# Performance work log

Measured on AMD Instinct MI355X. Metric: run time of the kernel, lower is better.

The kernel has to match this reference:

```python
import jax, jax.numpy as jnp
import numpy as np

N = 100000      # nodes
E = 1600000     # edges
G = 1024        # graphs in batch
H = 128         # graph_hidden
F_IN = 38
DEPTH = 4
EPS = 1e-5


def setup_inputs() -> dict:
    key = jax.random.key(0)
    ks = jax.random.split(key, 16)
    inp = {
        "h": jax.random.normal(ks[0], (N, F_IN), jnp.float32),
        "src": jax.random.randint(ks[1], (E,), 0, N, jnp.int32),
        "dst": jax.random.randint(ks[2], (E,), 0, N, jnp.int32),
        "node2graph": jnp.sort(jax.random.randint(ks[3], (N,), 0, G, jnp.int32)),
        "W1": jax.random.normal(ks[4], (F_IN, H), jnp.float32) * 0.1,
        "b1": jnp.zeros((H,), jnp.float32),
        "g1": jnp.ones((H,), jnp.float32),
        "be1": jnp.zeros((H,), jnp.float32),
        "W2s": jax.random.normal(ks[5], (DEPTH - 1, H, H), jnp.float32) * 0.1,
        "b2s": jnp.zeros((DEPTH - 1, H), jnp.float32),
        "g2s": jnp.ones((DEPTH - 1, H), jnp.float32),
        "be2s": jnp.zeros((DEPTH - 1, H), jnp.float32),
        "aw": jax.random.normal(ks[6], (H, 1), jnp.float32) * 0.1,
        "ab": jnp.zeros((1,), jnp.float32),
        "Wf1": jax.random.normal(ks[7], (H, 512), jnp.float32) * 0.1,
        "bf1": jnp.zeros((512,), jnp.float32),
        "gf1": jnp.ones((512,), jnp.float32),
        "bef1": jnp.zeros((512,), jnp.float32),
        "Wl": jax.random.normal(ks[8], (512, 256), jnp.float32) * 0.05,
        "bl": jnp.zeros((256,), jnp.float32),
        "gl": jnp.ones((256,), jnp.float32),
        "bel": jnp.zeros((256,), jnp.float32),
        "Wf2": jax.random.normal(ks[9], (256, 67), jnp.float32) * 0.05,
        "bf2": jnp.zeros((67,), jnp.float32),
    }
    return inp


def _bn(x, g, b):
    # BatchNorm1d in training mode: batch stats (biased variance), eps=1e-5.
    m = jnp.mean(x, axis=0)
    v = jnp.mean(jnp.square(x - m), axis=0)
    return g * (x - m) * jax.lax.rsqrt(v + EPS) + b


def reference(h, src, dst, node2graph,
              W1, b1, g1, be1, W2s, b2s, g2s, be2s,
              aw, ab, Wf1, bf1, gf1, bef1, Wl, bl, gl, bel, Wf2, bf2):
    ones_e = jnp.ones((E,), h.dtype)
    deg_out = jax.ops.segment_sum(ones_e, src, num_segments=N)
    deg_in = jax.ops.segment_sum(ones_e, dst, num_segments=N)
    ns = jax.lax.rsqrt(jnp.maximum(deg_out, 1.0))  # src-side D^{-1/2}
    nd = jax.lax.rsqrt(jnp.maximum(deg_in, 1.0))   # dst-side D^{-1/2}

    def gconv(x, W, b):
        # DGL GraphConv norm='both': D_dst^{-1/2} A D_src^{-1/2} x W + b
        msg = (x * ns[:, None])[src]                      # [E, F] gather
        agg = jax.ops.segment_sum(msg, dst, num_segments=N)
        return (agg * nd[:, None]) @ W + b

    # dropout p = 0.0 -> identity
    x = jax.nn.relu(_bn(gconv(h, W1, b1), g1, be1))
    for i in range(DEPTH - 1):
        x = jax.nn.relu(_bn(gconv(x, W2s[i], b2s[i]), g2s[i], be2s[i]))

    # WeightAndSum readout: sigmoid-gated segment sum over nodes per graph
    atom_weights = x @ aw + ab                            # [N, 1] (pre-sigmoid, returned)
    w = jax.nn.sigmoid(atom_weights)
    hg = jax.ops.segment_sum(x * w, node2graph, num_segments=G)  # [G, H]

    y = jax.nn.relu(_bn(hg @ Wf1 + bf1, gf1, bef1))
    y = jax.nn.relu(_bn(y @ Wl + bl, gl, bel))
    y = jax.nn.sigmoid(y @ Wf2 + bf2)                     # [G, 67]
    return (y, atom_weights)
```

## Files before the change

### kernel.cpp

```cpp
#include <hip/hip_runtime.h>
#include <math.h>

#define NN 100000
#define NE 1600000
#define NG 1024
#define MAXDEG 64
#define EPSB 1e-5f

#define NBUK 1563
#define NBLK 256
#define EPB  6250
#define FLAT (2*NBUK*NBLK)
#define NCH  ((FLAT + 1023)/1024)

typedef _Float16 h16;
typedef __attribute__((ext_vector_type(2))) _Float16 h16x2;
typedef __attribute__((ext_vector_type(4))) _Float16 h16x4;
typedef __attribute__((ext_vector_type(8))) _Float16 h16x8;
typedef __attribute__((ext_vector_type(4))) float f32x4;

static __device__ __forceinline__ float sigmoidf_(float x){ return 1.f/(1.f+__expf(-x)); }

__global__ __launch_bounds__(256)
void k_hist(const int* __restrict__ src, const int* __restrict__ dst,
            int* __restrict__ blockHist){
  __shared__ int hd[NBUK];
  __shared__ int hs[NBUK];
  int b = blockIdx.x, t = threadIdx.x;
  for (int j = t; j < NBUK; j += 256){ hd[j] = 0; hs[j] = 0; }
  __syncthreads();
  int e0 = b*EPB, e1 = e0 + EPB;
  for (int i = e0 + t; i < e1; i += 256){
    atomicAdd(&hd[dst[i]>>6], 1);
    atomicAdd(&hs[src[i]>>6], 1);
  }
  __syncthreads();
  for (int j = t; j < NBUK; j += 256){
    blockHist[(size_t)j*NBLK + b] = hd[j];
    blockHist[(size_t)(NBUK + j)*NBLK + b] = hs[j];
  }
}

__global__ __launch_bounds__(256)
void k_scan1(int* __restrict__ data, int* __restrict__ csum){
  __shared__ int s[256];
  int blk = blockIdx.x, t = threadIdx.x;
  int base = blk*1024 + t*4;
  int v0=0,v1=0,v2=0,v3=0;
  if (base+0 < FLAT) v0 = data[base+0];
  if (base+1 < FLAT) v1 = data[base+1];
  if (base+2 < FLAT) v2 = data[base+2];
  if (base+3 < FLAT) v3 = data[base+3];
  int tot = v0+v1+v2+v3;
  s[t] = tot; __syncthreads();
  for (int o=1;o<256;o<<=1){ int x = (t>=o)? s[t-o]:0; __syncthreads(); s[t]+=x; __syncthreads(); }
  int excl = s[t] - tot;
  if (t == 255) csum[blk] = s[255];
  if (base+0 < FLAT) data[base+0] = excl;
  if (base+1 < FLAT) data[base+1] = excl + v0;
  if (base+2 < FLAT) data[base+2] = excl + v0 + v1;
  if (base+3 < FLAT) data[base+3] = excl + v0 + v1 + v2;
}

__global__ void k_scan2(int* __restrict__ csum){
  __shared__ int s[1024];
  int t = threadIdx.x;
  int x = (t < NCH) ? csum[t] : 0;
  s[t] = x; __syncthreads();
  for (int o=1;o<1024;o<<=1){ int y = (t>=o)? s[t-o]:0; __syncthreads(); s[t]+=y; __syncthreads(); }
  if (t < NCH) csum[t] = s[t] - x;
}

__global__ __launch_bounds__(256)
void k_scan3(int* __restrict__ data, const int* __restrict__ csum){
  int blk = blockIdx.x, t = threadIdx.x;
  int add = csum[blk];
  int base = blk*1024 + t*4;
  if (base+0 < FLAT) data[base+0] += add;
  if (base+1 < FLAT) data[base+1] += add;
  if (base+2 < FLAT) data[base+2] += add;
  if (base+3 < FLAT) data[base+3] += add;
}

__global__ __launch_bounds__(256)
void k_scatter(const int* __restrict__ src, const int* __restrict__ dst,
               const int* __restrict__ scanned, unsigned int* __restrict__ sortedBuf){
  __shared__ int bd[NBUK];
  __shared__ int bs[NBUK];
  int b = blockIdx.x, t = threadIdx.x;
  for (int j = t; j < NBUK; j += 256){
    bd[j] = scanned[(size_t)j*NBLK + b];
    bs[j] = scanned[(size_t)(NBUK + j)*NBLK + b];
  }
  __syncthreads();
  int e0 = b*EPB, e1 = e0 + EPB;
  for (int i = e0 + t; i < e1; i += 256){
    int s = src[i], d = dst[i];
    int posD = atomicAdd(&bd[d>>6], 1);
    sortedBuf[posD] = (unsigned int)s | ((unsigned int)(d & 63) << 20);
    int posS = atomicAdd(&bs[s>>6], 1);
    sortedBuf[posS] = (unsigned int)s;
  }
}

__global__ __launch_bounds__(256)
void k_build(const unsigned int* __restrict__ sortedBuf, const int* __restrict__ scanned,
             int* __restrict__ eidx, int* __restrict__ degI,
             float* __restrict__ ns, float* __restrict__ nd){
  __shared__ int cnt[64];
  int k = blockIdx.x, t = threadIdx.x;
  int v0 = k*64;
  int nv = NN - v0; if (nv > 64) nv = 64;
  if (t < 64) cnt[t] = 0;
  __syncthreads();
  int startD = scanned[(size_t)k*NBLK];
  int endD   = scanned[(size_t)(k+1)*NBLK];
  for (int i = startD + t; i < endD; i += 256){
    unsigned int u = sortedBuf[i];
    int lid = (int)(u >> 20);
    int slot = atomicAdd(&cnt[lid], 1);
    if (slot < MAXDEG) eidx[(size_t)(v0 + lid)*MAXDEG + slot] = (int)(u & 0xFFFFFu);
  }
  __syncthreads();
  if (t < nv){
    int v = v0 + t;
    int dI = cnt[t];
    degI[v] = dI;
    nd[v] = rsqrtf(fmaxf((float)dI, 1.f));
    int c = dI > MAXDEG ? MAXDEG : dI;
    int ad = (c + 7) & ~7; if (ad < 8) ad = 8; if (ad > MAXDEG) ad = MAXDEG;
    for (int i = c; i < ad; i++) eidx[(size_t)v*MAXDEG + i] = NN;
  }
  __syncthreads();
  if (t < 64) cnt[t] = 0;
  __syncthreads();
  int startS = scanned[(size_t)(NBUK + k)*NBLK];
  int endS   = (k+1 < NBUK) ? scanned[(size_t)(NBUK + k + 1)*NBLK] : 2*NE;
  for (int i = startS + t; i < endS; i += 256){
    atomicAdd(&cnt[sortedBuf[i] & 63u], 1);
  }
  __syncthreads();
  if (t < nv) ns[v0 + t] = rsqrtf(fmaxf((float)cnt[t], 1.f));
}

__global__ void k_prepg(const int* __restrict__ n2g,
                        int* __restrict__ gs, int* __restrict__ ge, float* __restrict__ stats,
                        float* __restrict__ ns, h16* __restrict__ XA, h16* __restrict__ XB){
  int v = blockIdx.x*256 + threadIdx.x;
  if (v < NN){
    int g = n2g[v];
    if (v == 0){
      for (int q = 0; q <= g; q++) gs[q] = 0;
      for (int q = 0; q < g; q++) ge[q] = 0;
    } else {
      int gp = n2g[v-1];
      if (gp != g){
        for (int q = gp+1; q <= g; q++) gs[q] = v;
        for (int q = gp; q < g; q++) ge[q] = v;
      }
    }
    if (v == NN-1){
      for (int q = g+1; q < NG; q++) gs[q] = NN;
      for (int q = g; q < NG; q++) ge[q] = NN;
    }
  }
  if (v == NN) ns[NN] = 0.f;
  if (blockIdx.x == 0){
    int t = threadIdx.x;
    for (int j = t; j < 4096; j += 256) stats[j] = 0.f;
    if (t < 128){ XA[(size_t)NN*128 + t] = (h16)0.f; XB[(size_t)NN*128 + t] = (h16)0.f; }
  }
}

__global__ void k_convall(const float* __restrict__ W1, const float* __restrict__ W2s,
                          const float* __restrict__ Wf1, const float* __restrict__ Wl,
                          h16* __restrict__ W1t, h16* __restrict__ W2t,
                          h16* __restrict__ Wf1t, h16* __restrict__ Wlt){
  int i = blockIdx.x*256 + threadIdx.x;
  if (i < 8192){
    int c = i >> 6, k = i & 63;
    W1t[i] = (k < 38) ? (h16)W1[(size_t)k*128 + c] : (h16)0.f;
  } else if (i < 57344){
    int j = i - 8192; int l = j >> 14; int r = j & 16383;
    int c = r >> 7, k = r & 127;
    W2t[j] = (h16)W2s[(size_t)l*16384 + (size_t)k*128 + c];
  } else if (i < 122880){
    int j = i - 57344; int c = j >> 7, k = j & 127;
    Wf1t[j] = (h16)Wf1[(size_t)k*512 + c];
  } else if (i < 253952){
    int j = i - 122880; int c = j >> 9, k = j & 511;
    Wlt[j] = (h16)Wl[(size_t)k*256 + c];
  }
}

__global__ void k_prep1(const float* __restrict__ h, const float* __restrict__ ns,
                        h16* __restrict__ hn){
  int i = blockIdx.x*256 + threadIdx.x;
  if (i >= (NN+1)*40) return;
  int v = i / 40, c = i - v*40;
  float val = (v < NN && c < 38) ? h[(size_t)v*38 + c]*ns[v] : 0.f;
  hn[i] = (h16)val;
}

__global__ __launch_bounds__(256)
void k_gs40(const h16* __restrict__ hn, const int* __restrict__ eidx,
            const int* __restrict__ degI, const float* __restrict__ nd,
            h16* __restrict__ A38){
  int v = (blockIdx.x*256 + threadIdx.x) >> 6;
  int lane = threadIdx.x & 63;
  if (v >= NN) return;
  int deg = degI[v]; if (deg > MAXDEG) deg = MAXDEG;
  int deg8 = (deg + 7) & ~7; if (deg8 < 8) deg8 = 8; if (deg8 > MAXDEG) deg8 = MAXDEG;
  const int* row = eidx + v*MAXDEG;
  int g = lane / 20;
  int c0 = 2*(lane % 20);
  bool act = (lane < 40);
  int gg = g & 1;
  float a0 = 0.f, a1 = 0.f;
  int4 s4 = *(const int4*)(row + 4*gg);
  h16x2 u0={}, u1={}, u2={}, u3={};
  if (act){
    u0 = *(const h16x2*)(hn + (size_t)s4.x*40 + c0);
    u1 = *(const h16x2*)(hn + (size_t)s4.y*40 + c0);
    u2 = *(const h16x2*)(hn + (size_t)s4.z*40 + c0);
    u3 = *(const h16x2*)(hn + (size_t)s4.w*40 + c0);
  }
  for (int e = 0; e < deg8; e += 8){
    int nx = (e + 8 < deg8) ? e + 8 : e;
    int4 s4n = *(const int4*)(row + nx + 4*gg);
    h16x2 n0={}, n1={}, n2={}, n3={};
    if (act){
      n0 = *(const h16x2*)(hn + (size_t)s4n.x*40 + c0);
      n1 = *(const h16x2*)(hn + (size_t)s4n.y*40 + c0);
      n2 = *(const h16x2*)(hn + (size_t)s4n.z*40 + c0);
      n3 = *(const h16x2*)(hn + (size_t)s4n.w*40 + c0);
    }
    a0 += ((float)u0[0] + (float)u1[0]) + ((float)u2[0] + (float)u3[0]);
    a1 += ((float)u0[1] + (float)u1[1]) + ((float)u2[1] + (float)u3[1]);
    u0=n0; u1=n1; u2=n2; u3=n3;
  }
  float b0 = __shfl(a0, lane + 20);
  float b1 = __shfl(a1, lane + 20);
  if (lane < 20){
    float ndv = nd[v];
    h16x2 o; o[0] = (h16)((a0 + b0)*ndv); o[1] = (h16)((a1 + b1)*ndv);
    *(h16x2*)(A38 + (size_t)v*64 + c0) = o;
  } else if (lane < 32){
    h16x2 o; o[0] = (h16)0.f; o[1] = (h16)0.f;
    *(h16x2*)(A38 + (size_t)v*64 + 40 + 2*(lane - 20)) = o;
  }
}

__global__ __launch_bounds__(256)
void k_gs128(const h16* __restrict__ X, const int* __restrict__ eidx,
             const int* __restrict__ degI, const float* __restrict__ ns,
             const float* __restrict__ nd, const float* __restrict__ stats,
             const float* __restrict__ gam, const float* __restrict__ bet,
             h16* __restrict__ agg){
  __shared__ float scs[128], shs[128];
  int t = threadIdx.x;
  if (t < 128){
    float m = stats[t]*(1.f/(float)NN);
    float var = fmaxf(stats[128+t]*(1.f/(float)NN) - m*m, 0.f);
    float inv = rsqrtf(var + EPSB);
    float sc = gam[t]*inv;
    scs[t] = sc; shs[t] = fmaf(-sc, m, bet[t]);
  }
  __syncthreads();
  int v = (blockIdx.x*256 + t) >> 6;
  int lane = t & 63;
  if (v >= NN) return;
  int deg = degI[v]; if (deg > MAXDEG) deg = MAXDEG;
  int deg8 = (deg + 7) & ~7; if (deg8 < 8) deg8 = 8; if (deg8 > MAXDEG) deg8 = MAXDEG;
  const int* row = eidx + v*MAXDEG;
  int half = lane >> 5;
  int c0 = 4*(lane & 31);
  float4 sc = *(const float4*)&scs[c0];
  float4 sh = *(const float4*)&shs[c0];
  float a0=0.f, a1=0.f, a2=0.f, a3=0.f;
  int4 s4 = *(const int4*)(row + 4*half);
  float w0=ns[s4.x], w1=ns[s4.y], w2=ns[s4.z], w3=ns[s4.w];
  h16x4 u0 = *(const h16x4*)(X + (size_t)s4.x*128 + c0);
  h16x4 u1 = *(const h16x4*)(X + (size_t)s4.y*128 + c0);
  h16x4 u2 = *(const h16x4*)(X + (size_t)s4.z*128 + c0);
  h16x4 u3 = *(const h16x4*)(X + (size_t)s4.w*128 + c0);
  for (int e = 0; e < deg8; e += 8){
    int nx = (e + 8 < deg8) ? e + 8 : e;
    int4 s4n = *(const int4*)(row + nx + 4*half);
    float v0=ns[s4n.x], v1=ns[s4n.y], v2=ns[s4n.z], v3=ns[s4n.w];
    h16x4 n0 = *(const h16x4*)(X + (size_t)s4n.x*128 + c0);
    h16x4 n1 = *(const h16x4*)(X + (size_t)s4n.y*128 + c0);
    h16x4 n2 = *(const h16x4*)(X + (size_t)s4n.z*128 + c0);
    h16x4 n3 = *(const h16x4*)(X + (size_t)s4n.w*128 + c0);
    a0 = fmaf(fmaxf(fmaf((float)u0[0], sc.x, sh.x), 0.f), w0, a0);
    a1 = fmaf(fmaxf(fmaf((float)u0[1], sc.y, sh.y), 0.f), w0, a1);
    a2 = fmaf(fmaxf(fmaf((float)u0[2], sc.z, sh.z), 0.f), w0, a2);
    a3 = fmaf(fmaxf(fmaf((float)u0[3], sc.w, sh.w), 0.f), w0, a3);
    a0 = fmaf(fmaxf(fmaf((float)u1[0], sc.x, sh.x), 0.f), w1, a0);
    a1 = fmaf(fmaxf(fmaf((float)u1[1], sc.y, sh.y), 0.f), w1, a1);
    a2 = fmaf(fmaxf(fmaf((float)u1[2], sc.z, sh.z), 0.f), w1, a2);
    a3 = fmaf(fmaxf(fmaf((float)u1[3], sc.w, sh.w), 0.f), w1, a3);
    a0 = fmaf(fmaxf(fmaf((float)u2[0], sc.x, sh.x), 0.f), w2, a0);
    a1 = fmaf(fmaxf(fmaf((float)u2[1], sc.y, sh.y), 0.f), w2, a1);
    a2 = fmaf(fmaxf(fmaf((float)u2[2], sc.z, sh.z), 0.f), w2, a2);
    a3 = fmaf(fmaxf(fmaf((float)u2[3], sc.w, sh.w), 0.f), w2, a3);
    a0 = fmaf(fmaxf(fmaf((float)u3[0], sc.x, sh.x), 0.f), w3, a0);
    a1 = fmaf(fmaxf(fmaf((float)u3[1], sc.y, sh.y), 0.f), w3, a1);
    a2 = fmaf(fmaxf(fmaf((float)u3[2], sc.z, sh.z), 0.f), w3, a2);
    a3 = fmaf(fmaxf(fmaf((float)u3[3], sc.w, sh.w), 0.f), w3, a3);
    u0=n0; u1=n1; u2=n2; u3=n3;
    w0=v0; w1=v1; w2=v2; w3=v3;
  }
  a0 += __shfl_xor(a0, 32);
  a1 += __shfl_xor(a1, 32);
  a2 += __shfl_xor(a2, 32);
  a3 += __shfl_xor(a3, 32);
  if (half == 0){
    float ndv = nd[v];
    h16x4 o;
    o[0] = (h16)(a0*ndv); o[1] = (h16)(a1*ndv);
    o[2] = (h16)(a2*ndv); o[3] = (h16)(a3*ndv);
    *(h16x4*)(agg + (size_t)v*128 + c0) = o;
  }
}

__global__ __launch_bounds__(256)
void k_mgemm(const h16* __restrict__ A, const h16* __restrict__ Wt,
             const float* __restrict__ bias, h16* __restrict__ Cout,
             float* __restrict__ stats, int M, int K, int Nc){
  __shared__ h16 As[128][72];
  __shared__ h16 Bs[128][72];
  __shared__ float sred[2][128];
  int m0 = blockIdx.x*128, n0 = blockIdx.y*128;
  int t = threadIdx.x, w = t>>6, lane = t&63;
  int wr = (w>>1)*64, wc = (w&1)*64;
  f32x4 acc[4][4] = {};

  int ar = t>>3;
  int ac = (t&7)*8;
  for (int k0=0; k0<K; k0+=64){
    #pragma unroll
    for (int rr=0; rr<128; rr+=32){
      int gm = m0 + ar + rr;
      h16x8 val = {};
      if (gm < M) val = *(const h16x8*)(A + (size_t)gm*K + k0 + ac);
      *(h16x8*)&As[ar+rr][ac] = val;
    }
    #pragma unroll
    for (int rr=0; rr<128; rr+=32){
      int gc = n0 + ar + rr;
      h16x8 val = {};
      if (gc < Nc) val = *(const h16x8*)(Wt + (size_t)gc*K + k0 + ac);
      *(h16x8*)&Bs[ar+rr][ac] = val;
    }
    __syncthreads();
    int rsel = lane & 15;
    #pragma unroll
    for (int kk=0; kk<64; kk+=32){
      int ksel = kk + (lane>>4)*8;
      h16x8 af[4], bfr[4];
      #pragma unroll
      for (int i=0;i<4;i++) af[i]  = *(const h16x8*)&As[wr + i*16 + rsel][ksel];
      #pragma unroll
      for (int j=0;j<4;j++) bfr[j] = *(const h16x8*)&Bs[wc + j*16 + rsel][ksel];
      #pragma unroll
      for (int i=0;i<4;i++)
        #pragma unroll
        for (int j=0;j<4;j++)
          acc[i][j] = __builtin_amdgcn_mfma_f32_16x16x32_f16(af[i], bfr[j], acc[i][j], 0, 0, 0);
    }
    __syncthreads();
  }

  float csum[4] = {}, csq[4] = {};
  int colsel = lane & 15, rowsel = (lane>>4)*4;
  #pragma unroll
  for (int j=0;j<4;j++){
    int gc = n0 + wc + j*16 + colsel;
    float bv = (gc < Nc) ? bias[gc] : 0.f;
    #pragma unroll
    for (int i=0;i<4;i++){
      #pragma unroll
      for (int r=0;r<4;r++){
        int gm = m0 + wr + i*16 + rowsel + r;
        if (gm < M && gc < Nc){
          float v = acc[i][j][r] + bv;
          Cout[(size_t)gm*Nc + gc] = (h16)v;
          csum[j] += v; csq[j] += v*v;
        }
      }
    }
  }
  if (stats){
    ((float*)sred)[t] = 0.f;
    __syncthreads();
    #pragma unroll
    for (int j=0;j<4;j++){
      int lc = wc + j*16 + colsel;
      atomicAdd(&sred[0][lc], csum[j]);
      atomicAdd(&sred[1][lc], csq[j]);
    }
    __syncthreads();
    if (t < 128){
      int gc = n0 + t;
      if (gc < Nc){
        atomicAdd(&stats[gc],      sred[0][t]);
        atomicAdd(&stats[Nc + gc], sred[1][t]);
      }
    }
  }
}

__global__ __launch_bounds__(256)
void k_readout(const h16* __restrict__ X, const float* __restrict__ stats,
               const float* __restrict__ gam, const float* __restrict__ bet,
               const float* __restrict__ aw, const float* __restrict__ ab,
               const int* __restrict__ gs, const int* __restrict__ ge,
               float* __restrict__ awout, h16* __restrict__ hg){
  __shared__ float scs[128], shs[128], awv[128];
  __shared__ float red[4][128];
  int t = threadIdx.x;
  if (t < 128){
    float m = stats[t]*(1.f/(float)NN);
    float var = fmaxf(stats[128+t]*(1.f/(float)NN) - m*m, 0.f);
    float inv = rsqrtf(var + EPSB);
    float sc = gam[t]*inv;
    scs[t] = sc; shs[t] = fmaf(-sc, m, bet[t]);
    awv[t] = aw[t];
  }
  __syncthreads();
  int g = blockIdx.x;
  int s = gs[g], e = ge[g];
  int w = t>>6, lane = t&63, c0 = 2*lane;
  float sc0=scs[c0], sc1=scs[c0+1], sh0=shs[c0], sh1=shs[c0+1];
  float aw0=awv[c0], aw1=awv[c0+1];
  float ab0 = ab[0];
  float acc0=0.f, acc1=0.f;
  for (int n = s + w; n < e; n += 4){
    h16x2 u = *(const h16x2*)(X + (size_t)n*128 + c0);
    float x0 = fmaxf(fmaf((float)u[0], sc0, sh0), 0.f);
    float x1 = fmaxf(fmaf((float)u[1], sc1, sh1), 0.f);
    float d = x0*aw0 + x1*aw1;
    #pragma unroll
    for (int o=32;o>0;o>>=1) d += __shfl_xor(d, o);
    float tv = d + ab0;
    if (lane == 0) awout[n] = tv;
    float wn = sigmoidf_(tv);
    acc0 = fmaf(x0, wn, acc0);
    acc1 = fmaf(x1, wn, acc1);
  }
  red[w][c0] = acc0; red[w][c0+1] = acc1;
  __syncthreads();
  if (w == 0){
    float a0 = red[0][c0] + red[1][c0] + red[2][c0] + red[3][c0];
    float a1 = red[0][c0+1] + red[1][c0+1] + red[2][c0+1] + red[3][c0+1];
    h16x2 o; o[0] = (h16)a0; o[1] = (h16)a1;
    *(h16x2*)(hg + (size_t)g*128 + c0) = o;
  }
}

__global__ __launch_bounds__(256)
void k_bnapply_f(const h16* __restrict__ X, h16* __restrict__ Y,
                 const float* __restrict__ stats, const float* __restrict__ gam,
                 const float* __restrict__ bet, float invM, int C, int totalPairs){
  __shared__ float scs[512], shs[512];
  int t = threadIdx.x;
  for (int c = t; c < C; c += 256){
    float m = stats[c]*invM;
    float var = fmaxf(stats[C+c]*invM - m*m, 0.f);
    float inv = rsqrtf(var + EPSB);
    float sc = gam[c]*inv;
    scs[c] = sc; shs[c] = fmaf(-sc, m, bet[c]);
  }
  __syncthreads();
  int i = blockIdx.x*256 + t;
  if (i >= totalPairs) return;
  int pm = (C >> 1) - 1;
  int c0 = 2*(i & pm);
  h16x2 u = *(const h16x2*)(X + 2*(size_t)i);
  float x0 = fmaxf(fmaf((float)u[0], scs[c0],   shs[c0]),   0.f);
  float x1 = fmaxf(fmaf((float)u[1], scs[c0+1], shs[c0+1]), 0.f);
  h16x2 o; o[0] = (h16)x0; o[1] = (h16)x1;
  *(h16x2*)(Y + 2*(size_t)i) = o;
}

__global__ void k_final(const h16* __restrict__ y2, const float* __restrict__ Wf2,
                        const float* __restrict__ bf2v, float* __restrict__ out){
  int idx = blockIdx.x*256 + threadIdx.x;
  if (idx >= NG*67) return;
  int g = idx / 67, c = idx % 67;
  float s = bf2v[c];
  const h16* row = y2 + (size_t)g*256;
  for (int k=0;k<256;k+=2){
    h16x2 u = *(const h16x2*)(row + k);
    s = fmaf((float)u[0], Wf2[(size_t)k*67 + c], s);
    s = fmaf((float)u[1], Wf2[(size_t)(k+1)*67 + c], s);
  }
  out[(size_t)g*67 + c] = sigmoidf_(s);
}

extern "C" void kernel_launch(void* const* d_in, const int* in_sizes, int n_in,
                              void* d_out, int out_size, void* d_ws, size_t ws_size,
                              hipStream_t stream){
  const float* h   = (const float*)d_in[0];
  const int*   src = (const int*)d_in[1];
  const int*   dst = (const int*)d_in[2];
  const int*   n2g = (const int*)d_in[3];
  const float* W1  = (const float*)d_in[4];
  const float* b1  = (const float*)d_in[5];
  const float* g1  = (const float*)d_in[6];
  const float* be1 = (const float*)d_in[7];
  const float* W2s = (const float*)d_in[8];
  const float* b2s = (const float*)d_in[9];
  const float* g2s = (const float*)d_in[10];
  const float* be2s= (const float*)d_in[11];
  const float* aw  = (const float*)d_in[12];
  const float* ab  = (const float*)d_in[13];
  const float* Wf1 = (const float*)d_in[14];
  const float* bf1 = (const float*)d_in[15];
  const float* gf1 = (const float*)d_in[16];
  const float* bef1= (const float*)d_in[17];
  const float* Wl  = (const float*)d_in[18];
  const float* bl  = (const float*)d_in[19];
  const float* gl  = (const float*)d_in[20];
  const float* bel = (const float*)d_in[21];
  const float* Wf2 = (const float*)d_in[22];
  const float* bf2v= (const float*)d_in[23];
  float* out = (float*)d_out;

  char* p = (char*)d_ws;
  auto carve = [&](size_t bytes)->void*{
    void* r = (void*)p; p += (bytes + 255) & ~(size_t)255; return r;
  };
  h16* XA   = (h16*)carve((size_t)(NN+1)*128*2);
  h16* XB   = (h16*)carve((size_t)(NN+1)*128*2);
  h16* hn   = (h16*)carve((size_t)(NN+1)*40*2);
  h16* A38  = (h16*)carve((size_t)NN*64*2);
  int* eidx = (int*)carve((size_t)NN*MAXDEG*4);
  unsigned int* sortedBuf = (unsigned int*)carve((size_t)2*NE*4);
  int* blockHist = (int*)carve((size_t)FLAT*4);
  int* csum = (int*)carve(1024*4);
  int* degI = (int*)carve((size_t)NN*4);
  float* ns = (float*)carve((size_t)(NN+1)*4);
  float* nd = (float*)carve((size_t)NN*4);
  int* gsge = (int*)carve((size_t)2*NG*4);
  h16* hg   = (h16*)carve((size_t)NG*128*2);
  h16* y1p  = (h16*)carve((size_t)NG*512*2);
  h16* y1   = (h16*)carve((size_t)NG*512*2);
  h16* y2p  = (h16*)carve((size_t)NG*256*2);
  h16* y2   = (h16*)carve((size_t)NG*256*2);
  float* stats = (float*)carve(4096*4);
  h16* W1t  = (h16*)carve((size_t)128*64*2);
  h16* W2t  = (h16*)carve((size_t)3*128*128*2);
  h16* Wf1t = (h16*)carve((size_t)512*128*2);
  h16* Wlt  = (h16*)carve((size_t)256*512*2);

  int* gs = gsge;
  int* ge = gsge + NG;
  float* st1  = stats;
  float* st2a = stats + 256;
  float* st2b = stats + 512;
  float* st2c = stats + 768;
  float* stf1 = stats + 1024;
  float* stl  = stats + 2048;
  float* st2[3] = { st2a, st2b, st2c };

  k_convall<<<(253952+255)/256, 256, 0, stream>>>(W1, W2s, Wf1, Wl, W1t, W2t, Wf1t, Wlt);
  k_prepg  <<<(NN+1+255)/256, 256, 0, stream>>>(n2g, gs, ge, stats, ns, XA, XB);

  k_hist   <<<NBLK, 256, 0, stream>>>(src, dst, blockHist);
  k_scan1  <<<NCH, 256, 0, stream>>>(blockHist, csum);
  k_scan2  <<<1, 1024, 0, stream>>>(csum);
  k_scan3  <<<NCH, 256, 0, stream>>>(blockHist, csum);
  k_scatter<<<NBLK, 256, 0, stream>>>(src, dst, blockHist, sortedBuf);
  k_build  <<<NBUK, 256, 0, stream>>>(sortedBuf, blockHist, eidx, degI, ns, nd);

  const int nodeBlocks = (NN + 3)/4;
  const int gemmBlocks = (NN + 127)/128;

  k_prep1<<<((NN+1)*40+255)/256, 256, 0, stream>>>(h, ns, hn);
  k_gs40 <<<nodeBlocks, 256, 0, stream>>>(hn, eidx, degI, nd, A38);
  k_mgemm<<<dim3(gemmBlocks,1), 256, 0, stream>>>(A38, W1t, b1, XA, st1, NN, 64, 128);

  const float* stPrev[3] = { st1, st2a, st2b };
  const float* gPrev[3]  = { g1, g2s, g2s + 128 };
  const float* bePrev[3] = { be1, be2s, be2s + 128 };
  for (int i=0;i<3;i++){
    k_gs128<<<nodeBlocks, 256, 0, stream>>>(XA, eidx, degI, ns, nd,
                                            stPrev[i], gPrev[i], bePrev[i], XB);
    k_mgemm<<<dim3(gemmBlocks,1), 256, 0, stream>>>(XB, W2t + (size_t)i*128*128, b2s + i*128,
                                                    XA, st2[i], NN, 128, 128);
  }

  k_readout<<<NG, 256, 0, stream>>>(XA, st2c, g2s + 256, be2s + 256, aw, ab,
                                    gs, ge, out + (size_t)NG*67, hg);

  k_mgemm<<<dim3(NG/128, 4), 256, 0, stream>>>(hg, Wf1t, bf1, y1p, stf1, NG, 128, 512);
  k_bnapply_f<<<(NG*256+255)/256, 256, 0, stream>>>(y1p, y1, stf1, gf1, bef1,
                                                    1.0f/(float)NG, 512, NG*256);
  k_mgemm<<<dim3(NG/128, 2), 256, 0, stream>>>(y1, Wlt, bl, y2p, stl, NG, 512, 256);
  k_bnapply_f<<<(NG*128+255)/256, 256, 0, stream>>>(y2p, y2, stl, gl, bel,
                                                    1.0f/(float)NG, 256, NG*128);
  k_final<<<(NG*67+255)/256, 256, 0, stream>>>(y2, Wf2, bf2v, out);
}
```

Before: 654.0 us.

## Remap gather-sum kernels to half-wave per node with 16-byte loads

The gather-aggregate kernels now assign 32 lanes per node instead of 64. Each lane loads 8 (or 4) fp16 channels with one wide load, and two edge groups are merged by a shuffle. The BN-affine plus ReLU on gathered features is done with packed fp16 FMA/max, and the padding of eidx rows drops from multiples of 8 to multiples of 4. The input feature buffer is padded from 40 to 64 columns so loads are aligned. This cuts wasted padding edges and idle lanes and doubles nodes per block. The cost is more loop iterations per lane, and the BN affine is now computed in half precision, which loses some accuracy. The launch also assumes NN is divisible by 8.

```diff
diff --git a/kernel.cpp b/kernel.cpp
--- a/kernel.cpp
+++ b/kernel.cpp
@@ -20,6 +20,12 @@
 typedef __attribute__((ext_vector_type(4))) float f32x4;
 
 static __device__ __forceinline__ float sigmoidf_(float x){ return 1.f/(1.f+__expf(-x)); }
+static __device__ __forceinline__ unsigned int pkh(float a, float b){
+  h16 ha = (h16)a, hb = (h16)b;
+  unsigned short ua = __builtin_bit_cast(unsigned short, ha);
+  unsigned short ub = __builtin_bit_cast(unsigned short, hb);
+  return (unsigned int)ua | ((unsigned int)ub << 16);
+}
 
 __global__ __launch_bounds__(256)
 void k_hist(const int* __restrict__ src, const int* __restrict__ dst,
@@ -128,7 +134,7 @@
     degI[v] = dI;
     nd[v] = rsqrtf(fmaxf((float)dI, 1.f));
     int c = dI > MAXDEG ? MAXDEG : dI;
-    int ad = (c + 7) & ~7; if (ad < 8) ad = 8; if (ad > MAXDEG) ad = MAXDEG;
+    int ad = (c + 3) & ~3; if (ad < 4) ad = 4; if (ad > MAXDEG) ad = MAXDEG;
     for (int i = c; i < ad; i++) eidx[(size_t)v*MAXDEG + i] = NN;
   }
   __syncthreads();
@@ -196,8 +202,8 @@
 __global__ void k_prep1(const float* __restrict__ h, const float* __restrict__ ns,
                         h16* __restrict__ hn){
   int i = blockIdx.x*256 + threadIdx.x;
-  if (i >= (NN+1)*40) return;
-  int v = i / 40, c = i - v*40;
+  if (i >= (NN+1)*64) return;
+  int v = i >> 6, c = i & 63;
   float val = (v < NN && c < 38) ? h[(size_t)v*38 + c]*ns[v] : 0.f;
   hn[i] = (h16)val;
 }
@@ -206,48 +212,39 @@
 void k_gs40(const h16* __restrict__ hn, const int* __restrict__ eidx,
             const int* __restrict__ degI, const float* __restrict__ nd,
             h16* __restrict__ A38){
-  int v = (blockIdx.x*256 + threadIdx.x) >> 6;
-  int lane = threadIdx.x & 63;
-  if (v >= NN) return;
+  int t = threadIdx.x;
+  int lane = t & 63;
+  int eg = (lane >> 4) & 1;
+  int cl = lane & 15;
+  int c0 = cl*4;
+  int v = (blockIdx.x*256 + t) >> 5;
   int deg = degI[v]; if (deg > MAXDEG) deg = MAXDEG;
-  int deg8 = (deg + 7) & ~7; if (deg8 < 8) deg8 = 8; if (deg8 > MAXDEG) deg8 = MAXDEG;
-  const int* row = eidx + v*MAXDEG;
-  int g = lane / 20;
-  int c0 = 2*(lane % 20);
-  bool act = (lane < 40);
-  int gg = g & 1;
-  float a0 = 0.f, a1 = 0.f;
-  int4 s4 = *(const int4*)(row + 4*gg);
-  h16x2 u0={}, u1={}, u2={}, u3={};
-  if (act){
-    u0 = *(const h16x2*)(hn + (size_t)s4.x*40 + c0);
-    u1 = *(const h16x2*)(hn + (size_t)s4.y*40 + c0);
-    u2 = *(const h16x2*)(hn + (size_t)s4.z*40 + c0);
-    u3 = *(const h16x2*)(hn + (size_t)s4.w*40 + c0);
-  }
-  for (int e = 0; e < deg8; e += 8){
-    int nx = (e + 8 < deg8) ? e + 8 : e;
-    int4 s4n = *(const int4*)(row + nx + 4*gg);
-    h16x2 n0={}, n1={}, n2={}, n3={};
-    if (act){
-      n0 = *(const h16x2*)(hn + (size_t)s4n.x*40 + c0);
-      n1 = *(const h16x2*)(hn + (size_t)s4n.y*40 + c0);
-      n2 = *(const h16x2*)(hn + (size_t)s4n.z*40 + c0);
-      n3 = *(const h16x2*)(hn + (size_t)s4n.w*40 + c0);
-    }
-    a0 += ((float)u0[0] + (float)u1[0]) + ((float)u2[0] + (float)u3[0]);
-    a1 += ((float)u0[1] + (float)u1[1]) + ((float)u2[1] + (float)u3[1]);
-    u0=n0; u1=n1; u2=n2; u3=n3;
-  }
-  float b0 = __shfl(a0, lane + 20);
-  float b1 = __shfl(a1, lane + 20);
-  if (lane < 20){
+  int deg4 = (deg + 3) & ~3; if (deg4 < 4) deg4 = 4; if (deg4 > MAXDEG) deg4 = MAXDEG;
+  const int* row = eidx + (size_t)v*MAXDEG;
+  float a0=0.f, a1=0.f, a2=0.f, a3=0.f;
+  int s = row[eg];
+  uint2 xw = *(const uint2*)(hn + (size_t)s*64 + c0);
+  for (int e = 0; e < deg4; e += 2){
+    int en = e + 2;
+    int ec = (en < deg4) ? en : e;
+    int s2 = row[ec + eg];
+    uint2 xw2 = *(const uint2*)(hn + (size_t)s2*64 + c0);
+    h16x2 pa = __builtin_bit_cast(h16x2, xw.x);
+    h16x2 pb = __builtin_bit_cast(h16x2, xw.y);
+    a0 += (float)pa[0]; a1 += (float)pa[1];
+    a2 += (float)pb[0]; a3 += (float)pb[1];
+    xw = xw2;
+  }
+  a0 += __shfl_xor(a0, 16);
+  a1 += __shfl_xor(a1, 16);
+  a2 += __shfl_xor(a2, 16);
+  a3 += __shfl_xor(a3, 16);
+  if (eg == 0){
     float ndv = nd[v];
-    h16x2 o; o[0] = (h16)((a0 + b0)*ndv); o[1] = (h16)((a1 + b1)*ndv);
-    *(h16x2*)(A38 + (size_t)v*64 + c0) = o;
-  } else if (lane < 32){
-    h16x2 o; o[0] = (h16)0.f; o[1] = (h16)0.f;
-    *(h16x2*)(A38 + (size_t)v*64 + 40 + 2*(lane - 20)) = o;
+    uint2 o;
+    o.x = pkh(a0*ndv, a1*ndv);
+    o.y = pkh(a2*ndv, a3*ndv);
+    *(uint2*)(A38 + (size_t)v*64 + c0) = o;
   }
 }
 
@@ -267,60 +264,52 @@
     scs[t] = sc; shs[t] = fmaf(-sc, m, bet[t]);
   }
   __syncthreads();
-  int v = (blockIdx.x*256 + t) >> 6;
   int lane = t & 63;
-  if (v >= NN) return;
+  int eg = (lane >> 4) & 1;
+  int cl = lane & 15;
+  int c0 = cl*8;
+  int v = (blockIdx.x*256 + t) >> 5;
+  h16x2 scp[4], shp[4], zz;
+  zz[0] = (h16)0.f; zz[1] = (h16)0.f;
+  #pragma unroll
+  for (int d=0; d<4; d++){
+    scp[d][0] = (h16)scs[c0+2*d]; scp[d][1] = (h16)scs[c0+2*d+1];
+    shp[d][0] = (h16)shs[c0+2*d]; shp[d][1] = (h16)shs[c0+2*d+1];
+  }
   int deg = degI[v]; if (deg > MAXDEG) deg = MAXDEG;
-  int deg8 = (deg + 7) & ~7; if (deg8 < 8) deg8 = 8; if (deg8 > MAXDEG) deg8 = MAXDEG;
-  const int* row = eidx + v*MAXDEG;
-  int half = lane >> 5;
-  int c0 = 4*(lane & 31);
-  float4 sc = *(const float4*)&scs[c0];
-  float4 sh = *(const float4*)&shs[c0];
-  float a0=0.f, a1=0.f, a2=0.f, a3=0.f;
-  int4 s4 = *(const int4*)(row + 4*half);
-  float w0=ns[s4.x], w1=ns[s4.y], w2=ns[s4.z], w3=ns[s4.w];
-  h16x4 u0 = *(const h16x4*)(X + (size_t)s4.x*128 + c0);
-  h16x4 u1 = *(const h16x4*)(X + (size_t)s4.y*128 + c0);
-  h16x4 u2 = *(const h16x4*)(X + (size_t)s4.z*128 + c0);
-  h16x4 u3 = *(const h16x4*)(X + (size_t)s4.w*128 + c0);
-  for (int e = 0; e < deg8; e += 8){
-    int nx = (e + 8 < deg8) ? e + 8 : e;
-    int4 s4n = *(const int4*)(row + nx + 4*half);
-    float v0=ns[s4n.x], v1=ns[s4n.y], v2=ns[s4n.z], v3=ns[s4n.w];
-    h16x4 n0 = *(const h16x4*)(X + (size_t)s4n.x*128 + c0);
-    h16x4 n1 = *(const h16x4*)(X + (size_t)s4n.y*128 + c0);
-    h16x4 n2 = *(const h16x4*)(X + (size_t)s4n.z*128 + c0);
-    h16x4 n3 = *(const h16x4*)(X + (size_t)s4n.w*128 + c0);
-    a0 = fmaf(fmaxf(fmaf((float)u0[0], sc.x, sh.x), 0.f), w0, a0);
-    a1 = fmaf(fmaxf(fmaf((float)u0[1], sc.y, sh.y), 0.f), w0, a1);
-    a2 = fmaf(fmaxf(fmaf((float)u0[2], sc.z, sh.z), 0.f), w0, a2);
-    a3 = fmaf(fmaxf(fmaf((float)u0[3], sc.w, sh.w), 0.f), w0, a3);
-    a0 = fmaf(fmaxf(fmaf((float)u1[0], sc.x, sh.x), 0.f), w1, a0);
-    a1 = fmaf(fmaxf(fmaf((float)u1[1], sc.y, sh.y), 0.f), w1, a1);
-    a2 = fmaf(fmaxf(fmaf((float)u1[2], sc.z, sh.z), 0.f), w1, a2);
-    a3 = fmaf(fmaxf(fmaf((float)u1[3], sc.w, sh.w), 0.f), w1, a3);
-    a0 = fmaf(fmaxf(fmaf((float)u2[0], sc.x, sh.x), 0.f), w2, a0);
-    a1 = fmaf(fmaxf(fmaf((float)u2[1], sc.y, sh.y), 0.f), w2, a1);
-    a2 = fmaf(fmaxf(fmaf((float)u2[2], sc.z, sh.z), 0.f), w2, a2);
-    a3 = fmaf(fmaxf(fmaf((float)u2[3], sc.w, sh.w), 0.f), w2, a3);
-    a0 = fmaf(fmaxf(fmaf((float)u3[0], sc.x, sh.x), 0.f), w3, a0);
-    a1 = fmaf(fmaxf(fmaf((float)u3[1], sc.y, sh.y), 0.f), w3, a1);
-    a2 = fmaf(fmaxf(fmaf((float)u3[2], sc.z, sh.z), 0.f), w3, a2);
-    a3 = fmaf(fmaxf(fmaf((float)u3[3], sc.w, sh.w), 0.f), w3, a3);
-    u0=n0; u1=n1; u2=n2; u3=n3;
-    w0=v0; w1=v1; w2=v2; w3=v3;
-  }
-  a0 += __shfl_xor(a0, 32);
-  a1 += __shfl_xor(a1, 32);
-  a2 += __shfl_xor(a2, 32);
-  a3 += __shfl_xor(a3, 32);
-  if (half == 0){
+  int deg4 = (deg + 3) & ~3; if (deg4 < 4) deg4 = 4; if (deg4 > MAXDEG) deg4 = MAXDEG;
+  const int* row = eidx + (size_t)v*MAXDEG;
+  float acc[8] = {};
+  int s = row[eg];
+  float nsf = ns[s];
+  uint4 xw = *(const uint4*)(X + (size_t)s*128 + c0);
+  for (int e = 0; e < deg4; e += 2){
+    int en = e + 2;
+    int ec = (en < deg4) ? en : e;
+    int s2 = row[ec + eg];
+    float ns2 = ns[s2];
+    uint4 xw2 = *(const uint4*)(X + (size_t)s2*128 + c0);
+    unsigned int ws[4] = { xw.x, xw.y, xw.z, xw.w };
+    #pragma unroll
+    for (int d=0; d<4; d++){
+      h16x2 xp = __builtin_bit_cast(h16x2, ws[d]);
+      h16x2 tt = __builtin_elementwise_fma(xp, scp[d], shp[d]);
+      tt = __builtin_elementwise_max(tt, zz);
+      acc[2*d]   = fmaf((float)tt[0], nsf, acc[2*d]);
+      acc[2*d+1] = fmaf((float)tt[1], nsf, acc[2*d+1]);
+    }
+    s = s2; nsf = ns2; xw = xw2;
+  }
+  #pragma unroll
+  for (int d=0; d<8; d++) acc[d] += __shfl_xor(acc[d], 16);
+  if (eg == 0){
     float ndv = nd[v];
-    h16x4 o;
-    o[0] = (h16)(a0*ndv); o[1] = (h16)(a1*ndv);
-    o[2] = (h16)(a2*ndv); o[3] = (h16)(a3*ndv);
-    *(h16x4*)(agg + (size_t)v*128 + c0) = o;
+    uint4 o;
+    o.x = pkh(acc[0]*ndv, acc[1]*ndv);
+    o.y = pkh(acc[2]*ndv, acc[3]*ndv);
+    o.z = pkh(acc[4]*ndv, acc[5]*ndv);
+    o.w = pkh(acc[6]*ndv, acc[7]*ndv);
+    *(uint4*)(agg + (size_t)v*128 + c0) = o;
   }
 }
 
@@ -534,7 +523,7 @@
   };
   h16* XA   = (h16*)carve((size_t)(NN+1)*128*2);
   h16* XB   = (h16*)carve((size_t)(NN+1)*128*2);
-  h16* hn   = (h16*)carve((size_t)(NN+1)*40*2);
+  h16* hn   = (h16*)carve((size_t)(NN+1)*64*2);
   h16* A38  = (h16*)carve((size_t)NN*64*2);
   int* eidx = (int*)carve((size_t)NN*MAXDEG*4);
   unsigned int* sortedBuf = (unsigned int*)carve((size_t)2*NE*4);
@@ -575,10 +564,10 @@
   k_scatter<<<NBLK, 256, 0, stream>>>(src, dst, blockHist, sortedBuf);
   k_build  <<<NBUK, 256, 0, stream>>>(sortedBuf, blockHist, eidx, degI, ns, nd);
 
-  const int nodeBlocks = (NN + 3)/4;
+  const int nodeBlocks = NN/8;
   const int gemmBlocks = (NN + 127)/128;
 
-  k_prep1<<<((NN+1)*40+255)/256, 256, 0, stream>>>(h, ns, hn);
+  k_prep1<<<((NN+1)*64+255)/256, 256, 0, stream>>>(h, ns, hn);
   k_gs40 <<<nodeBlocks, 256, 0, stream>>>(hn, eidx, degI, nd, A38);
   k_mgemm<<<dim3(gemmBlocks,1), 256, 0, stream>>>(A38, W1t, b1, XA, st1, NN, 64, 128);
 
```

Measured after the change: 677.6 us. 1.04x slower.

## Fuse scan fixup, input prep, and head batchnorms into neighboring kernels

Applied to the files above, without the earlier changes.

Drops the scan3 pass by adding the chunk offset when the scanned histogram is read in scatter and build. Folds the h*ns fp16 prep into k_build, using a 64-wide padded row layout for hn. Fuses the two head batchnorm-apply kernels into the following GEMM's A-load and into the final linear. Also doubles hist/scatter block size to 512. This removes several small launches and intermediate buffers, at the cost of redundant BN math per tile and a wider hn row that raises gather traffic.

```diff
diff --git a/kernel.cpp b/kernel.cpp
--- a/kernel.cpp
+++ b/kernel.cpp
@@ -21,21 +21,21 @@
 
 static __device__ __forceinline__ float sigmoidf_(float x){ return 1.f/(1.f+__expf(-x)); }
 
-__global__ __launch_bounds__(256)
+__global__ __launch_bounds__(512)
 void k_hist(const int* __restrict__ src, const int* __restrict__ dst,
             int* __restrict__ blockHist){
   __shared__ int hd[NBUK];
   __shared__ int hs[NBUK];
   int b = blockIdx.x, t = threadIdx.x;
-  for (int j = t; j < NBUK; j += 256){ hd[j] = 0; hs[j] = 0; }
+  for (int j = t; j < NBUK; j += 512){ hd[j] = 0; hs[j] = 0; }
   __syncthreads();
   int e0 = b*EPB, e1 = e0 + EPB;
-  for (int i = e0 + t; i < e1; i += 256){
+  for (int i = e0 + t; i < e1; i += 512){
     atomicAdd(&hd[dst[i]>>6], 1);
     atomicAdd(&hs[src[i]>>6], 1);
   }
   __syncthreads();
-  for (int j = t; j < NBUK; j += 256){
+  for (int j = t; j < NBUK; j += 512){
     blockHist[(size_t)j*NBLK + b] = hd[j];
     blockHist[(size_t)(NBUK + j)*NBLK + b] = hs[j];
   }
@@ -71,30 +71,24 @@
   if (t < NCH) csum[t] = s[t] - x;
 }
 
-__global__ __launch_bounds__(256)
-void k_scan3(int* __restrict__ data, const int* __restrict__ csum){
-  int blk = blockIdx.x, t = threadIdx.x;
-  int add = csum[blk];
-  int base = blk*1024 + t*4;
-  if (base+0 < FLAT) data[base+0] += add;
-  if (base+1 < FLAT) data[base+1] += add;
-  if (base+2 < FLAT) data[base+2] += add;
-  if (base+3 < FLAT) data[base+3] += add;
-}
-
-__global__ __launch_bounds__(256)
+static __device__ __forceinline__ int rd_scanned(const int* data, const int* csum, int idx){
+  return data[idx] + csum[idx >> 10];
+}
+
+__global__ __launch_bounds__(512)
 void k_scatter(const int* __restrict__ src, const int* __restrict__ dst,
-               const int* __restrict__ scanned, unsigned int* __restrict__ sortedBuf){
+               const int* __restrict__ scanned, const int* __restrict__ csum,
+               unsigned int* __restrict__ sortedBuf){
   __shared__ int bd[NBUK];
   __shared__ int bs[NBUK];
   int b = blockIdx.x, t = threadIdx.x;
-  for (int j = t; j < NBUK; j += 256){
-    bd[j] = scanned[(size_t)j*NBLK + b];
-    bs[j] = scanned[(size_t)(NBUK + j)*NBLK + b];
+  for (int j = t; j < NBUK; j += 512){
+    bd[j] = rd_scanned(scanned, csum, j*NBLK + b);
+    bs[j] = rd_scanned(scanned, csum, (NBUK + j)*NBLK + b);
   }
   __syncthreads();
   int e0 = b*EPB, e1 = e0 + EPB;
-  for (int i = e0 + t; i < e1; i += 256){
+  for (int i = e0 + t; i < e1; i += 512){
     int s = src[i], d = dst[i];
     int posD = atomicAdd(&bd[d>>6], 1);
     sortedBuf[posD] = (unsigned int)s | ((unsigned int)(d & 63) << 20);
@@ -105,16 +99,18 @@
 
 __global__ __launch_bounds__(256)
 void k_build(const unsigned int* __restrict__ sortedBuf, const int* __restrict__ scanned,
+             const int* __restrict__ csum, const float* __restrict__ h,
              int* __restrict__ eidx, int* __restrict__ degI,
-             float* __restrict__ ns, float* __restrict__ nd){
+             float* __restrict__ ns, float* __restrict__ nd, h16* __restrict__ hn){
   __shared__ int cnt[64];
+  __shared__ float nsl[64];
   int k = blockIdx.x, t = threadIdx.x;
   int v0 = k*64;
   int nv = NN - v0; if (nv > 64) nv = 64;
   if (t < 64) cnt[t] = 0;
   __syncthreads();
-  int startD = scanned[(size_t)k*NBLK];
-  int endD   = scanned[(size_t)(k+1)*NBLK];
+  int startD = rd_scanned(scanned, csum, k*NBLK);
+  int endD   = rd_scanned(scanned, csum, (k+1)*NBLK);
   for (int i = startD + t; i < endD; i += 256){
     unsigned int u = sortedBuf[i];
     int lid = (int)(u >> 20);
@@ -134,13 +130,32 @@
   __syncthreads();
   if (t < 64) cnt[t] = 0;
   __syncthreads();
-  int startS = scanned[(size_t)(NBUK + k)*NBLK];
-  int endS   = (k+1 < NBUK) ? scanned[(size_t)(NBUK + k + 1)*NBLK] : 2*NE;
+  int startS = rd_scanned(scanned, csum, (NBUK + k)*NBLK);
+  int endS   = (k+1 < NBUK) ? rd_scanned(scanned, csum, (NBUK + k + 1)*NBLK) : 2*NE;
   for (int i = startS + t; i < endS; i += 256){
     atomicAdd(&cnt[sortedBuf[i] & 63u], 1);
   }
   __syncthreads();
-  if (t < nv) ns[v0 + t] = rsqrtf(fmaxf((float)cnt[t], 1.f));
+  if (t < 64){
+    float nsv = 0.f;
+    if (t < nv){
+      nsv = rsqrtf(fmaxf((float)cnt[t], 1.f));
+      ns[v0 + t] = nsv;
+    }
+    nsl[t] = nsv;
+  }
+  __syncthreads();
+  for (int i = t; i < 64*64; i += 256){
+    int r = i >> 6, c = i & 63;
+    int v = v0 + r;
+    if (v < NN){
+      float val = (c < 38) ? h[(size_t)v*38 + c]*nsl[r] : 0.f;
+      hn[(size_t)v*64 + c] = (h16)val;
+    }
+  }
+  if (k == 0){
+    for (int i = t; i < 64; i += 256) hn[(size_t)NN*64 + i] = (h16)0.f;
+  }
 }
 
 __global__ void k_prepg(const int* __restrict__ n2g,
@@ -193,15 +208,6 @@
   }
 }
 
-__global__ void k_prep1(const float* __restrict__ h, const float* __restrict__ ns,
-                        h16* __restrict__ hn){
-  int i = blockIdx.x*256 + threadIdx.x;
-  if (i >= (NN+1)*40) return;
-  int v = i / 40, c = i - v*40;
-  float val = (v < NN && c < 38) ? h[(size_t)v*38 + c]*ns[v] : 0.f;
-  hn[i] = (h16)val;
-}
-
 __global__ __launch_bounds__(256)
 void k_gs40(const h16* __restrict__ hn, const int* __restrict__ eidx,
             const int* __restrict__ degI, const float* __restrict__ nd,
@@ -211,7 +217,7 @@
   if (v >= NN) return;
   int deg = degI[v]; if (deg > MAXDEG) deg = MAXDEG;
   int deg8 = (deg + 7) & ~7; if (deg8 < 8) deg8 = 8; if (deg8 > MAXDEG) deg8 = MAXDEG;
-  const int* row = eidx + v*MAXDEG;
+  const int* row = eidx + (size_t)v*MAXDEG;
   int g = lane / 20;
   int c0 = 2*(lane % 20);
   bool act = (lane < 40);
@@ -220,20 +226,20 @@
   int4 s4 = *(const int4*)(row + 4*gg);
   h16x2 u0={}, u1={}, u2={}, u3={};
   if (act){
-    u0 = *(const h16x2*)(hn + (size_t)s4.x*40 + c0);
-    u1 = *(const h16x2*)(hn + (size_t)s4.y*40 + c0);
-    u2 = *(const h16x2*)(hn + (size_t)s4.z*40 + c0);
-    u3 = *(const h16x2*)(hn + (size_t)s4.w*40 + c0);
+    u0 = *(const h16x2*)(hn + (size_t)s4.x*64 + c0);
+    u1 = *(const h16x2*)(hn + (size_t)s4.y*64 + c0);
+    u2 = *(const h16x2*)(hn + (size_t)s4.z*64 + c0);
+    u3 = *(const h16x2*)(hn + (size_t)s4.w*64 + c0);
   }
   for (int e = 0; e < deg8; e += 8){
     int nx = (e + 8 < deg8) ? e + 8 : e;
     int4 s4n = *(const int4*)(row + nx + 4*gg);
     h16x2 n0={}, n1={}, n2={}, n3={};
     if (act){
-      n0 = *(const h16x2*)(hn + (size_t)s4n.x*40 + c0);
-      n1 = *(const h16x2*)(hn + (size_t)s4n.y*40 + c0);
-      n2 = *(const h16x2*)(hn + (size_t)s4n.z*40 + c0);
-      n3 = *(const h16x2*)(hn + (size_t)s4n.w*40 + c0);
+      n0 = *(const h16x2*)(hn + (size_t)s4n.x*64 + c0);
+      n1 = *(const h16x2*)(hn + (size_t)s4n.y*64 + c0);
+      n2 = *(const h16x2*)(hn + (size_t)s4n.z*64 + c0);
+      n3 = *(const h16x2*)(hn + (size_t)s4n.w*64 + c0);
     }
     a0 += ((float)u0[0] + (float)u1[0]) + ((float)u2[0] + (float)u3[0]);
     a1 += ((float)u0[1] + (float)u1[1]) + ((float)u2[1] + (float)u3[1]);
@@ -272,7 +278,7 @@
   if (v >= NN) return;
   int deg = degI[v]; if (deg > MAXDEG) deg = MAXDEG;
   int deg8 = (deg + 7) & ~7; if (deg8 < 8) deg8 = 8; if (deg8 > MAXDEG) deg8 = MAXDEG;
-  const int* row = eidx + v*MAXDEG;
+  const int* row = eidx + (size_t)v*MAXDEG;
   int half = lane >> 5;
   int c0 = 4*(lane & 31);
   float4 sc = *(const float4*)&scs[c0];
@@ -412,6 +418,110 @@
 }
 
 __global__ __launch_bounds__(256)
+void k_mgemmbn(const h16* __restrict__ A, const h16* __restrict__ Wt,
+               const float* __restrict__ bias, h16* __restrict__ Cout,
+               float* __restrict__ statsOut, const float* __restrict__ statsIn,
+               const float* __restrict__ gam, const float* __restrict__ bet,
+               float invM, int M, int K, int Nc){
+  __shared__ float scs[512], shs[512];
+  __shared__ h16 As[128][72];
+  __shared__ h16 Bs[128][72];
+  __shared__ float sred[2][128];
+  int t = threadIdx.x;
+  for (int c = t; c < K; c += 256){
+    float m = statsIn[c]*invM;
+    float var = fmaxf(statsIn[K+c]*invM - m*m, 0.f);
+    float inv = rsqrtf(var + EPSB);
+    float sc = gam[c]*inv;
+    scs[c] = sc; shs[c] = fmaf(-sc, m, bet[c]);
+  }
+  __syncthreads();
+  int m0 = blockIdx.x*128, n0 = blockIdx.y*128;
+  int w = t>>6, lane = t&63;
+  int wr = (w>>1)*64, wc = (w&1)*64;
+  f32x4 acc[4][4] = {};
+
+  int ar = t>>3;
+  int ac = (t&7)*8;
+  for (int k0=0; k0<K; k0+=64){
+    #pragma unroll
+    for (int rr=0; rr<128; rr+=32){
+      int gm = m0 + ar + rr;
+      h16x8 val = {};
+      if (gm < M){
+        h16x8 raw = *(const h16x8*)(A + (size_t)gm*K + k0 + ac);
+        #pragma unroll
+        for (int j=0;j<8;j++){
+          int kk = k0 + ac + j;
+          val[j] = (h16)fmaxf(fmaf((float)raw[j], scs[kk], shs[kk]), 0.f);
+        }
+      }
+      *(h16x8*)&As[ar+rr][ac] = val;
+    }
+    #pragma unroll
+    for (int rr=0; rr<128; rr+=32){
+      int gc = n0 + ar + rr;
+      h16x8 val = {};
+      if (gc < Nc) val = *(const h16x8*)(Wt + (size_t)gc*K + k0 + ac);
+      *(h16x8*)&Bs[ar+rr][ac] = val;
+    }
+    __syncthreads();
+    int rsel = lane & 15;
+    #pragma unroll
+    for (int kk=0; kk<64; kk+=32){
+      int ksel = kk + (lane>>4)*8;
+      h16x8 af[4], bfr[4];
+      #pragma unroll
+      for (int i=0;i<4;i++) af[i]  = *(const h16x8*)&As[wr + i*16 + rsel][ksel];
+      #pragma unroll
+      for (int j=0;j<4;j++) bfr[j] = *(const h16x8*)&Bs[wc + j*16 + rsel][ksel];
+      #pragma unroll
+      for (int i=0;i<4;i++)
+        #pragma unroll
+        for (int j=0;j<4;j++)
+          acc[i][j] = __builtin_amdgcn_mfma_f32_16x16x32_f16(af[i], bfr[j], acc[i][j], 0, 0, 0);
+    }
+    __syncthreads();
+  }
+
+  float csum[4] = {}, csq[4] = {};
+  int colsel = lane & 15, rowsel = (lane>>4)*4;
+  #pragma unroll
+  for (int j=0;j<4;j++){
+    int gc = n0 + wc + j*16 + colsel;
+    float bv = (gc < Nc) ? bias[gc] : 0.f;
+    #pragma unroll
+    for (int i=0;i<4;i++){
+      #pragma unroll
+      for (int r=0;r<4;r++){
+        int gm = m0 + wr + i*16 + rowsel + r;
+        if (gm < M && gc < Nc){
+          float v = acc[i][j][r] + bv;
+          Cout[(size_t)gm*Nc + gc] = (h16)v;
+          csum[j] += v; csq[j] += v*v;
+        }
+      }
+    }
+  }
+  ((float*)sred)[t] = 0.f;
+  __syncthreads();
+  #pragma unroll
+  for (int j=0;j<4;j++){
+    int lc = wc + j*16 + colsel;
+    atomicAdd(&sred[0][lc], csum[j]);
+    atomicAdd(&sred[1][lc], csq[j]);
+  }
+  __syncthreads();
+  if (t < 128){
+    int gc = n0 + t;
+    if (gc < Nc){
+      atomicAdd(&statsOut[gc],      sred[0][t]);
+      atomicAdd(&statsOut[Nc + gc], sred[1][t]);
+    }
+  }
+}
+
+__global__ __launch_bounds__(256)
 void k_readout(const h16* __restrict__ X, const float* __restrict__ stats,
                const float* __restrict__ gam, const float* __restrict__ bet,
                const float* __restrict__ aw, const float* __restrict__ ab,
@@ -460,41 +570,31 @@
 }
 
 __global__ __launch_bounds__(256)
-void k_bnapply_f(const h16* __restrict__ X, h16* __restrict__ Y,
-                 const float* __restrict__ stats, const float* __restrict__ gam,
-                 const float* __restrict__ bet, float invM, int C, int totalPairs){
-  __shared__ float scs[512], shs[512];
+void k_finalbn(const h16* __restrict__ y2p, const float* __restrict__ Wf2,
+               const float* __restrict__ bf2v, const float* __restrict__ statsIn,
+               const float* __restrict__ gam, const float* __restrict__ bet,
+               float* __restrict__ out){
+  __shared__ float scs[256], shs[256];
   int t = threadIdx.x;
-  for (int c = t; c < C; c += 256){
-    float m = stats[c]*invM;
-    float var = fmaxf(stats[C+c]*invM - m*m, 0.f);
+  {
+    float m = statsIn[t]*(1.f/(float)NG);
+    float var = fmaxf(statsIn[256+t]*(1.f/(float)NG) - m*m, 0.f);
     float inv = rsqrtf(var + EPSB);
-    float sc = gam[c]*inv;
-    scs[c] = sc; shs[c] = fmaf(-sc, m, bet[c]);
-  }
-  __syncthreads();
-  int i = blockIdx.x*256 + t;
-  if (i >= totalPairs) return;
-  int pm = (C >> 1) - 1;
-  int c0 = 2*(i & pm);
-  h16x2 u = *(const h16x2*)(X + 2*(size_t)i);
-  float x0 = fmaxf(fmaf((float)u[0], scs[c0],   shs[c0]),   0.f);
-  float x1 = fmaxf(fmaf((float)u[1], scs[c0+1], shs[c0+1]), 0.f);
-  h16x2 o; o[0] = (h16)x0; o[1] = (h16)x1;
-  *(h16x2*)(Y + 2*(size_t)i) = o;
-}
-
-__global__ void k_final(const h16* __restrict__ y2, const float* __restrict__ Wf2,
-                        const float* __restrict__ bf2v, float* __restrict__ out){
-  int idx = blockIdx.x*256 + threadIdx.x;
+    float sc = gam[t]*inv;
+    scs[t] = sc; shs[t] = fmaf(-sc, m, bet[t]);
+  }
+  __syncthreads();
+  int idx = blockIdx.x*256 + t;
   if (idx >= NG*67) return;
   int g = idx / 67, c = idx % 67;
   float s = bf2v[c];
-  const h16* row = y2 + (size_t)g*256;
+  const h16* row = y2p + (size_t)g*256;
   for (int k=0;k<256;k+=2){
     h16x2 u = *(const h16x2*)(row + k);
-    s = fmaf((float)u[0], Wf2[(size_t)k*67 + c], s);
-    s = fmaf((float)u[1], Wf2[(size_t)(k+1)*67 + c], s);
+    float x0 = fmaxf(fmaf((float)u[0], scs[k],   shs[k]),   0.f);
+    float x1 = fmaxf(fmaf((float)u[1], scs[k+1], shs[k+1]), 0.f);
+    s = fmaf(x0, Wf2[(size_t)k*67 + c], s);
+    s = fmaf(x1, Wf2[(size_t)(k+1)*67 + c], s);
   }
   out[(size_t)g*67 + c] = sigmoidf_(s);
 }
@@ -534,7 +634,7 @@
   };
   h16* XA   = (h16*)carve((size_t)(NN+1)*128*2);
   h16* XB   = (h16*)carve((size_t)(NN+1)*128*2);
-  h16* hn   = (h16*)carve((size_t)(NN+1)*40*2);
+  h16* hn   = (h16*)carve((size_t)(NN+1)*64*2);
   h16* A38  = (h16*)carve((size_t)NN*64*2);
   int* eidx = (int*)carve((size_t)NN*MAXDEG*4);
   unsigned int* sortedBuf = (unsigned int*)carve((size_t)2*NE*4);
@@ -546,9 +646,7 @@
   int* gsge = (int*)carve((size_t)2*NG*4);
   h16* hg   = (h16*)carve((size_t)NG*128*2);
   h16* y1p  = (h16*)carve((size_t)NG*512*2);
-  h16* y1   = (h16*)carve((size_t)NG*512*2);
   h16* y2p  = (h16*)carve((size_t)NG*256*2);
-  h16* y2   = (h16*)carve((size_t)NG*256*2);
   float* stats = (float*)carve(4096*4);
   h16* W1t  = (h16*)carve((size_t)128*64*2);
   h16* W2t  = (h16*)carve((size_t)3*128*128*2);
@@ -568,17 +666,15 @@
   k_convall<<<(253952+255)/256, 256, 0, stream>>>(W1, W2s, Wf1, Wl, W1t, W2t, Wf1t, Wlt);
   k_prepg  <<<(NN+1+255)/256, 256, 0, stream>>>(n2g, gs, ge, stats, ns, XA, XB);
 
-  k_hist   <<<NBLK, 256, 0, stream>>>(src, dst, blockHist);
+  k_hist   <<<NBLK, 512, 0, stream>>>(src, dst, blockHist);
   k_scan1  <<<NCH, 256, 0, stream>>>(blockHist, csum);
   k_scan2  <<<1, 1024, 0, stream>>>(csum);
-  k_scan3  <<<NCH, 256, 0, stream>>>(blockHist, csum);
-  k_scatter<<<NBLK, 256, 0, stream>>>(src, dst, blockHist, sortedBuf);
-  k_build  <<<NBUK, 256, 0, stream>>>(sortedBuf, blockHist, eidx, degI, ns, nd);
+  k_scatter<<<NBLK, 512, 0, stream>>>(src, dst, blockHist, csum, sortedBuf);
+  k_build  <<<NBUK, 256, 0, stream>>>(sortedBuf, blockHist, csum, h, eidx, degI, ns, nd, hn);
 
   const int nodeBlocks = (NN + 3)/4;
   const int gemmBlocks = (NN + 127)/128;
 
-  k_prep1<<<((NN+1)*40+255)/256, 256, 0, stream>>>(h, ns, hn);
   k_gs40 <<<nodeBlocks, 256, 0, stream>>>(hn, eidx, degI, nd, A38);
   k_mgemm<<<dim3(gemmBlocks,1), 256, 0, stream>>>(A38, W1t, b1, XA, st1, NN, 64, 128);
 
@@ -595,11 +691,8 @@
   k_readout<<<NG, 256, 0, stream>>>(XA, st2c, g2s + 256, be2s + 256, aw, ab,
                                     gs, ge, out + (size_t)NG*67, hg);
 
-  k_mgemm<<<dim3(NG/128, 4), 256, 0, stream>>>(hg, Wf1t, bf1, y1p, stf1, NG, 128, 512);
-  k_bnapply_f<<<(NG*256+255)/256, 256, 0, stream>>>(y1p, y1, stf1, gf1, bef1,
-                                                    1.0f/(float)NG, 512, NG*256);
-  k_mgemm<<<dim3(NG/128, 2), 256, 0, stream>>>(y1, Wlt, bl, y2p, stl, NG, 512, 256);
-  k_bnapply_f<<<(NG*128+255)/256, 256, 0, stream>>>(y2p, y2, stl, gl, bel,
-                                                    1.0f/(float)NG, 256, NG*128);
-  k_final<<<(NG*67+255)/256, 256, 0, stream>>>(y2, Wf2, bf2v, out);
-}
+  k_mgemm  <<<dim3(NG/128, 4), 256, 0, stream>>>(hg, Wf1t, bf1, y1p, stf1, NG, 128, 512);
+  k_mgemmbn<<<dim3(NG/128, 2), 256, 0, stream>>>(y1p, Wlt, bl, y2p, stl, stf1, gf1, bef1,
+                                                 1.0f/(float)NG, NG, 512, 256);
+  k_finalbn<<<(NG*67+255)/256, 256, 0, stream>>>(y2p, Wf2, bf2v, stl, gl, bel, out);
+}
```

Result: no change. 650.4 us (-0.5%).
